# Kernel tuning notes

Measured on AMD Instinct MI355X. Metric: run time of the kernel, lower is better.

The kernel has to match this reference:

```python
import jax, jax.numpy as jnp
import numpy as np

TEMPERATURE = 8.0   # sqrt(d_k), d_k = 64
TOP_K = 5           # SparseAttention default top_k in mimicry/RIMs
EPS = 1e-7          # matches torch 10e-8


def _sparsify(attn_rows):
    """Per-row top-k sparsification: keep mass above the k-th largest value,
    clamp at zero, renormalize. attn_rows: [N, L]."""
    topk_vals = jax.lax.top_k(attn_rows, TOP_K)[0]          # [N, K]
    delta = topk_vals[:, -1:] + EPS                          # k-th largest per row
    w = jnp.maximum(attn_rows - delta, 0.0)                  # clamp(min=0)
    return w / (jnp.sum(w, axis=1, keepdims=True) + EPS)


def setup_inputs() -> dict:
    key = jax.random.key(0)
    kq, kk, kv = jax.random.split(key, 3)
    B, L, D = 4, 4096, 64
    q = jax.random.normal(kq, (B, L, D), dtype=jnp.float32)
    k = jax.random.normal(kk, (B, L, D), dtype=jnp.float32)
    v = jax.random.normal(kv, (B, L, D), dtype=jnp.float32)
    return {"q": q, "k": k, "v": v}


def reference(q, k, v):
    # attn = softmax(q k^T / temperature); dropout is identity in eval mode
    attn = jnp.einsum('bqd,bkd->bqk', q / TEMPERATURE, k)   # [B, Lq, Lk]
    attn = jax.nn.softmax(attn, axis=-1)
    B, Lq, Lk = attn.shape
    attn = _sparsify(attn.reshape(B * Lq, Lk)).reshape(B, Lq, Lk)
    out = jnp.einsum('bqk,bkd->bqd', attn, v)               # [B, Lq, Dv]
    return out, attn
```

## Files before the change

### kernel.cpp

```cpp
#include <hip/hip_runtime.h>
#include <math.h>

#define NB 4
#define L 4096
#define D 64
#define QPB 64
#define TCOLS 128
#define NT (L / TCOLS)

typedef __attribute__((ext_vector_type(8))) short short8;
typedef __attribute__((ext_vector_type(4))) float floatx4;
typedef unsigned int u32;

static __device__ inline ushort2 f2bf2(float x) {
    unsigned int u = __builtin_bit_cast(unsigned int, x);
    unsigned int uh = u + (0x7FFFu + ((u >> 16) & 1u));
    unsigned short h = (unsigned short)(uh >> 16);
    float hf = __builtin_bit_cast(float, (unsigned int)h << 16);
    float r = x - hf;
    unsigned int v = __builtin_bit_cast(unsigned int, r);
    unsigned short l = (unsigned short)((v + (0x7FFFu + ((v >> 16) & 1u))) >> 16);
    ushort2 p; p.x = h; p.y = l; return p;
}

static __device__ inline void dma16(const unsigned short* g, unsigned short* l) {
    __builtin_amdgcn_global_load_lds(
        (const __attribute__((address_space(1))) u32*)g,
        (__attribute__((address_space(3))) u32*)l, 16, 0, 0);
}

#define WS_QL 1048576
#define WS_KW 2097152

__global__ __launch_bounds__(256)
void convert_kernel(const float* __restrict__ qg, const float* __restrict__ kg,
                    unsigned short* __restrict__ ws) {
    unsigned int i = blockIdx.x * 256 + threadIdx.x;
    if (i < 262144) {
        float4 qv = ((const float4*)qg)[i];
        ushort2 p0 = f2bf2(qv.x), p1 = f2bf2(qv.y), p2 = f2bf2(qv.z), p3 = f2bf2(qv.w);
        ushort4 h; h.x = p0.x; h.y = p1.x; h.z = p2.x; h.w = p3.x;
        ushort4 l; l.x = p0.y; l.y = p1.y; l.z = p2.y; l.w = p3.y;
        *(ushort4*)&ws[i * 4] = h;
        *(ushort4*)&ws[WS_QL + i * 4] = l;
    } else {
        unsigned int j = i - 262144;
        float4 kv = ((const float4*)kg)[j];
        ushort2 p0 = f2bf2(kv.x), p1 = f2bf2(kv.y), p2 = f2bf2(kv.z), p3 = f2bf2(kv.w);
        ushort4 h; h.x = p0.x; h.y = p1.x; h.z = p2.x; h.w = p3.x;
        ushort4 l; l.x = p0.y; l.y = p1.y; l.z = p2.y; l.w = p3.y;
        unsigned int bcol = j >> 4;
        unsigned int f4   = j & 15;
        unsigned int tile = bcol >> 7;
        unsigned int tcol = bcol & 127;
        unsigned int cq   = f4 >> 1, half = f4 & 1;
        unsigned int base = tile * 16384 + (cq * 128 + tcol) * 8 + half * 4;
        *(ushort4*)&ws[WS_KW + base] = h;
        *(ushort4*)&ws[WS_KW + base + 8192] = l;
    }
}

__global__ __launch_bounds__(512, 2)
void sparse_attn_kernel(const unsigned short* __restrict__ ws,
                        const float* __restrict__ vg,
                        float* __restrict__ outg) {
    __shared__ unsigned short skt[2][16384];
    __shared__ float smv[QPB][5];
    __shared__ int   smc[QPB][5];
    __shared__ float smz[QPB];

    const int tid  = threadIdx.x;
    const int lane = tid & 63;
    const int w    = tid >> 6;
    const int rg   = w & 3;
    const int ch   = w >> 2;
    const int c16  = lane & 15;
    const int quad = lane >> 4;

    const int sblk  = (blockIdx.x & 7) * 32 + (blockIdx.x >> 3);
    const int qbase = sblk * QPB;
    const int b     = qbase >> 12;

    const unsigned short* qh = ws;
    const unsigned short* ql = ws + WS_QL;
    const unsigned short* kw = ws + WS_KW + (size_t)b * NT * 16384;

    const float* vb = vg + (size_t)b * L * D;
    float* attng = outg + (size_t)NB * L * D;
    float4* zrow = (float4*)(attng + (size_t)qbase * L);

    const int qrow = qbase + rg * 16 + c16;
    const short8 a0h = *(const short8*)&qh[(size_t)qrow * 64 + quad * 8];
    const short8 a1h = *(const short8*)&qh[(size_t)qrow * 64 + 32 + quad * 8];
    const short8 a0l = *(const short8*)&ql[(size_t)qrow * 64 + quad * 8];
    const short8 a1l = *(const short8*)&ql[(size_t)qrow * 64 + 32 + quad * 8];

#pragma unroll
    for (int jj = 0; jj < 4; ++jj) {
        int idx = w * 4 + jj;
        dma16(kw + idx * 512 + lane * 8, &skt[0][idx * 512]);
    }
    __syncthreads();

    float Z[4] = {0.f, 0.f, 0.f, 0.f};
    float tv[4][5];
    int   tc[4][5];
#pragma unroll
    for (int r = 0; r < 4; ++r)
#pragma unroll
        for (int i = 0; i < 5; ++i) { tv[r][i] = -INFINITY; tc[r][i] = -1; }

    for (int g = 0; g < NT; ++g) {
        if (g + 1 < NT) {
#pragma unroll
            for (int jj = 0; jj < 4; ++jj) {
                int idx = w * 4 + jj;
                dma16(kw + (g + 1) * 16384 + idx * 512 + lane * 8,
                      &skt[(g + 1) & 1][idx * 512]);
            }
        }

        const unsigned short* kbh = skt[g & 1];
        const unsigned short* kbl = skt[g & 1] + 8192;

#pragma unroll
        for (int j = 0; j < 4; ++j) {
            const int cg = ch * 4 + j;
            const int cb = cg * 16 + c16;
            short8 b0h = *(const short8*)&kbh[((quad)     * 128 + cb) * 8];
            short8 b1h = *(const short8*)&kbh[((4 + quad) * 128 + cb) * 8];
            short8 b0l = *(const short8*)&kbl[((quad)     * 128 + cb) * 8];
            short8 b1l = *(const short8*)&kbl[((4 + quad) * 128 + cb) * 8];
            floatx4 acc = {0.f, 0.f, 0.f, 0.f};
            acc = __builtin_amdgcn_mfma_f32_16x16x32_bf16(a0h, b0h, acc, 0, 0, 0);
            acc = __builtin_amdgcn_mfma_f32_16x16x32_bf16(a1h, b1h, acc, 0, 0, 0);
            acc = __builtin_amdgcn_mfma_f32_16x16x32_bf16(a0l, b0h, acc, 0, 0, 0);
            acc = __builtin_amdgcn_mfma_f32_16x16x32_bf16(a1l, b1h, acc, 0, 0, 0);
            acc = __builtin_amdgcn_mfma_f32_16x16x32_bf16(a0h, b0l, acc, 0, 0, 0);
            acc = __builtin_amdgcn_mfma_f32_16x16x32_bf16(a1h, b1l, acc, 0, 0, 0);
            const int col = g * TCOLS + cb;
#pragma unroll
            for (int r = 0; r < 4; ++r) {
                float s = acc[r] * 0.125f;
                Z[r] += __expf(s);
                bool q0 = s > tv[r][0];
                bool q1 = s > tv[r][1];
                bool q2 = s > tv[r][2];
                bool q3 = s > tv[r][3];
                bool q4 = s > tv[r][4];
                tv[r][4] = q4 ? (q3 ? tv[r][3] : s)   : tv[r][4];
                tc[r][4] = q4 ? (q3 ? tc[r][3] : col) : tc[r][4];
                tv[r][3] = q3 ? (q2 ? tv[r][2] : s)   : tv[r][3];
                tc[r][3] = q3 ? (q2 ? tc[r][2] : col) : tc[r][3];
                tv[r][2] = q2 ? (q1 ? tv[r][1] : s)   : tv[r][2];
                tc[r][2] = q2 ? (q1 ? tc[r][1] : col) : tc[r][2];
                tv[r][1] = q1 ? (q0 ? tv[r][0] : s)   : tv[r][1];
                tc[r][1] = q1 ? (q0 ? tc[r][0] : col) : tc[r][1];
                tv[r][0] = q0 ? s   : tv[r][0];
                tc[r][0] = q0 ? col : tc[r][0];
            }
        }

        float4 zv = make_float4(0.f, 0.f, 0.f, 0.f);
#pragma unroll
        for (int jj = 0; jj < 4; ++jj)
            zrow[(size_t)g * 2048 + jj * 512 + tid] = zv;

        __syncthreads();
    }

    float gv[4][5]; int gc[4][5]; float zz[4];
#pragma unroll
    for (int r = 0; r < 4; ++r) {
        float z = Z[r];
        z += __shfl_xor(z, 1, 64);
        z += __shfl_xor(z, 2, 64);
        z += __shfl_xor(z, 4, 64);
        z += __shfl_xor(z, 8, 64);
        zz[r] = z;
        const int rowl = rg * 16 + quad * 4 + r;
#pragma unroll
        for (int k5 = 0; k5 < 5; ++k5) {
            float cv = tv[r][0]; int cc = tc[r][0];
#pragma unroll
            for (int m = 8; m >= 1; m >>= 1) {
                float ov = __shfl_xor(cv, m, 64);
                int   oc = __shfl_xor(cc, m, 64);
                if (ov > cv || (ov == cv && oc < cc)) { cv = ov; cc = oc; }
            }
            gv[r][k5] = cv; gc[r][k5] = cc;
            if (ch == 1 && c16 == k5) { smv[rowl][k5] = cv; smc[rowl][k5] = cc; }
            if (tc[r][0] == cc) {
                tv[r][0] = tv[r][1]; tc[r][0] = tc[r][1];
                tv[r][1] = tv[r][2]; tc[r][1] = tc[r][2];
                tv[r][2] = tv[r][3]; tc[r][2] = tc[r][3];
                tv[r][3] = tv[r][4]; tc[r][3] = tc[r][4];
                tv[r][4] = -INFINITY; tc[r][4] = -1;
            }
        }
        if (ch == 1 && c16 == 5) smz[rowl] = z;
    }
    __syncthreads();

    if (ch == 0) {
#pragma unroll
        for (int r = 0; r < 4; ++r) {
            const int rowl = rg * 16 + quad * 4 + r;
            float z = zz[r] + smz[rowl];
#pragma unroll
            for (int f = 0; f < 5; ++f) {
                float fv = smv[rowl][f];
                int   fc = smc[rowl][f];
                bool q0 = fv > gv[r][0];
                bool q1 = fv > gv[r][1];
                bool q2 = fv > gv[r][2];
                bool q3 = fv > gv[r][3];
                bool q4 = fv > gv[r][4];
                gv[r][4] = q4 ? (q3 ? gv[r][3] : fv) : gv[r][4];
                gc[r][4] = q4 ? (q3 ? gc[r][3] : fc) : gc[r][4];
                gv[r][3] = q3 ? (q2 ? gv[r][2] : fv) : gv[r][3];
                gc[r][3] = q3 ? (q2 ? gc[r][2] : fc) : gc[r][3];
                gv[r][2] = q2 ? (q1 ? gv[r][1] : fv) : gv[r][2];
                gc[r][2] = q2 ? (q1 ? gc[r][1] : fc) : gc[r][2];
                gv[r][1] = q1 ? (q0 ? gv[r][0] : fv) : gv[r][1];
                gc[r][1] = q1 ? (q0 ? gc[r][0] : fc) : gc[r][1];
                gv[r][0] = q0 ? fv : gv[r][0];
                gc[r][0] = q0 ? fc : gc[r][0];
            }

            float invz = 1.0f / z;
            float e0 = __expf(gv[r][0]) * invz;
            float e1 = __expf(gv[r][1]) * invz;
            float e2 = __expf(gv[r][2]) * invz;
            float e3 = __expf(gv[r][3]) * invz;
            float e4 = __expf(gv[r][4]) * invz;
            float delta = e4 + 1e-7f;
            float w0 = fmaxf(e0 - delta, 0.f);
            float w1 = fmaxf(e1 - delta, 0.f);
            float w2 = fmaxf(e2 - delta, 0.f);
            float w3 = fmaxf(e3 - delta, 0.f);
            float inv = 1.0f / (w0 + w1 + w2 + w3 + 1e-7f);
            w0 *= inv; w1 *= inv; w2 *= inv; w3 *= inv;

            const int rowabs = qbase + rowl;

            const float4 v0 = *(const float4*)(vb + (size_t)gc[r][0] * D + c16 * 4);
            const float4 v1 = *(const float4*)(vb + (size_t)gc[r][1] * D + c16 * 4);
            const float4 v2 = *(const float4*)(vb + (size_t)gc[r][2] * D + c16 * 4);
            const float4 v3 = *(const float4*)(vb + (size_t)gc[r][3] * D + c16 * 4);
            float4 o;
            o.x = w0 * v0.x + w1 * v1.x + w2 * v2.x + w3 * v3.x;
            o.y = w0 * v0.y + w1 * v1.y + w2 * v2.y + w3 * v3.y;
            o.z = w0 * v0.z + w1 * v1.z + w2 * v2.z + w3 * v3.z;
            o.w = w0 * v0.w + w1 * v1.w + w2 * v2.w + w3 * v3.w;
            *(float4*)(outg + (size_t)rowabs * D + c16 * 4) = o;

            if (c16 < 4) {
                float wv = c16 == 0 ? w0 : c16 == 1 ? w1 : c16 == 2 ? w2 : w3;
                int   cs = c16 == 0 ? gc[r][0] : c16 == 1 ? gc[r][1]
                         : c16 == 2 ? gc[r][2] : gc[r][3];
                attng[(size_t)rowabs * L + cs] = wv;
            }
        }
    }
}

extern "C" void kernel_launch(void* const* d_in, const int* in_sizes, int n_in,
                              void* d_out, int out_size, void* d_ws, size_t ws_size,
                              hipStream_t stream) {
    const float* q = (const float*)d_in[0];
    const float* k = (const float*)d_in[1];
    const float* v = (const float*)d_in[2];
    float* out = (float*)d_out;
    unsigned short* ws = (unsigned short*)d_ws;

    convert_kernel<<<2048, 256, 0, stream>>>(q, k, ws);

    dim3 grid(NB * L / QPB);
    sparse_attn_kernel<<<grid, 512, 0, stream>>>(ws, v, out);
}
```

Before: 346.5 us.

## Drop softmax denominator via exp ratio, read K directly from global, shrink blocks

Folds log2(e)/temperature into Q during conversion so scores come out in log2 units. The sparsified weights are then computed as (2^(s_i - s_5) - 1) normalized, which removes the per-element exp and row-sum accumulation entirely. The shared-memory K double buffer is replaced with direct global loads from a K layout with per-batch column-major chunks. Blocks shrink to 16 query rows with four waves splitting the columns, followed by an LDS merge of the per-wave top-5 lists. This drops per-element exp and index bookkeeping and barriers, but relies on cache hits for K reuse and changes the EPS semantics slightly.

Result: faster. 334.9 us (-3.4%).

```diff
diff --git a/kernel.cpp b/kernel.cpp
--- a/kernel.cpp
+++ b/kernel.cpp
@@ -4,13 +4,14 @@
 #define NB 4
 #define L 4096
 #define D 64
-#define QPB 64
-#define TCOLS 128
-#define NT (L / TCOLS)
+#define WS_QL 1048576
+#define WS_K  2097152
+#define KBS   524288
+#define KPL   262144
+#define QSCALE 0.1803368801111243f
 
 typedef __attribute__((ext_vector_type(8))) short short8;
 typedef __attribute__((ext_vector_type(4))) float floatx4;
-typedef unsigned int u32;
 
 static __device__ inline ushort2 f2bf2(float x) {
     unsigned int u = __builtin_bit_cast(unsigned int, x);
@@ -23,22 +24,14 @@
     ushort2 p; p.x = h; p.y = l; return p;
 }
 
-static __device__ inline void dma16(const unsigned short* g, unsigned short* l) {
-    __builtin_amdgcn_global_load_lds(
-        (const __attribute__((address_space(1))) u32*)g,
-        (__attribute__((address_space(3))) u32*)l, 16, 0, 0);
-}
-
-#define WS_QL 1048576
-#define WS_KW 2097152
-
 __global__ __launch_bounds__(256)
 void convert_kernel(const float* __restrict__ qg, const float* __restrict__ kg,
                     unsigned short* __restrict__ ws) {
     unsigned int i = blockIdx.x * 256 + threadIdx.x;
     if (i < 262144) {
         float4 qv = ((const float4*)qg)[i];
-        ushort2 p0 = f2bf2(qv.x), p1 = f2bf2(qv.y), p2 = f2bf2(qv.z), p3 = f2bf2(qv.w);
+        ushort2 p0 = f2bf2(qv.x * QSCALE), p1 = f2bf2(qv.y * QSCALE),
+                p2 = f2bf2(qv.z * QSCALE), p3 = f2bf2(qv.w * QSCALE);
         ushort4 h; h.x = p0.x; h.y = p1.x; h.z = p2.x; h.w = p3.x;
         ushort4 l; l.x = p0.y; l.y = p1.y; l.z = p2.y; l.w = p3.y;
         *(ushort4*)&ws[i * 4] = h;
@@ -51,136 +44,106 @@
         ushort4 l; l.x = p0.y; l.y = p1.y; l.z = p2.y; l.w = p3.y;
         unsigned int bcol = j >> 4;
         unsigned int f4   = j & 15;
-        unsigned int tile = bcol >> 7;
-        unsigned int tcol = bcol & 127;
+        unsigned int b    = bcol >> 12, col = bcol & 4095;
         unsigned int cq   = f4 >> 1, half = f4 & 1;
-        unsigned int base = tile * 16384 + (cq * 128 + tcol) * 8 + half * 4;
-        *(ushort4*)&ws[WS_KW + base] = h;
-        *(ushort4*)&ws[WS_KW + base + 8192] = l;
-    }
-}
-
-__global__ __launch_bounds__(512, 2)
+        size_t base = WS_K + (size_t)b * KBS + ((size_t)cq * 4096 + col) * 8 + half * 4;
+        *(ushort4*)&ws[base] = h;
+        *(ushort4*)&ws[base + KPL] = l;
+    }
+}
+
+#define SENT 0x7FFFFFFF
+
+__global__ __launch_bounds__(256, 4)
 void sparse_attn_kernel(const unsigned short* __restrict__ ws,
                         const float* __restrict__ vg,
                         float* __restrict__ outg) {
-    __shared__ unsigned short skt[2][16384];
-    __shared__ float smv[QPB][5];
-    __shared__ int   smc[QPB][5];
-    __shared__ float smz[QPB];
+    __shared__ float smv[3][16][5];
+    __shared__ int   smc[3][16][4];
 
     const int tid  = threadIdx.x;
     const int lane = tid & 63;
-    const int w    = tid >> 6;
-    const int rg   = w & 3;
-    const int ch   = w >> 2;
+    const int wid  = tid >> 6;
     const int c16  = lane & 15;
     const int quad = lane >> 4;
 
-    const int sblk  = (blockIdx.x & 7) * 32 + (blockIdx.x >> 3);
-    const int qbase = sblk * QPB;
+    const int sblk  = (blockIdx.x & 7) * 128 + (blockIdx.x >> 3);
+    const int qbase = sblk * 16;
     const int b     = qbase >> 12;
 
-    const unsigned short* qh = ws;
-    const unsigned short* ql = ws + WS_QL;
-    const unsigned short* kw = ws + WS_KW + (size_t)b * NT * 16384;
-
+    const unsigned short* qh   = ws;
+    const unsigned short* ql   = ws + WS_QL;
+    const unsigned short* kbat = ws + WS_K + (size_t)b * KBS;
     const float* vb = vg + (size_t)b * L * D;
     float* attng = outg + (size_t)NB * L * D;
-    float4* zrow = (float4*)(attng + (size_t)qbase * L);
-
-    const int qrow = qbase + rg * 16 + c16;
+
+    const int qrow = qbase + c16;
     const short8 a0h = *(const short8*)&qh[(size_t)qrow * 64 + quad * 8];
     const short8 a1h = *(const short8*)&qh[(size_t)qrow * 64 + 32 + quad * 8];
     const short8 a0l = *(const short8*)&ql[(size_t)qrow * 64 + quad * 8];
     const short8 a1l = *(const short8*)&ql[(size_t)qrow * 64 + 32 + quad * 8];
 
-#pragma unroll
-    for (int jj = 0; jj < 4; ++jj) {
-        int idx = w * 4 + jj;
-        dma16(kw + idx * 512 + lane * 8, &skt[0][idx * 512]);
-    }
-    __syncthreads();
-
-    float Z[4] = {0.f, 0.f, 0.f, 0.f};
     float tv[4][5];
-    int   tc[4][5];
-#pragma unroll
-    for (int r = 0; r < 4; ++r)
-#pragma unroll
-        for (int i = 0; i < 5; ++i) { tv[r][i] = -INFINITY; tc[r][i] = -1; }
-
-    for (int g = 0; g < NT; ++g) {
-        if (g + 1 < NT) {
-#pragma unroll
-            for (int jj = 0; jj < 4; ++jj) {
-                int idx = w * 4 + jj;
-                dma16(kw + (g + 1) * 16384 + idx * 512 + lane * 8,
-                      &skt[(g + 1) & 1][idx * 512]);
-            }
-        }
-
-        const unsigned short* kbh = skt[g & 1];
-        const unsigned short* kbl = skt[g & 1] + 8192;
-
-#pragma unroll
-        for (int j = 0; j < 4; ++j) {
-            const int cg = ch * 4 + j;
-            const int cb = cg * 16 + c16;
-            short8 b0h = *(const short8*)&kbh[((quad)     * 128 + cb) * 8];
-            short8 b1h = *(const short8*)&kbh[((4 + quad) * 128 + cb) * 8];
-            short8 b0l = *(const short8*)&kbl[((quad)     * 128 + cb) * 8];
-            short8 b1l = *(const short8*)&kbl[((4 + quad) * 128 + cb) * 8];
-            floatx4 acc = {0.f, 0.f, 0.f, 0.f};
-            acc = __builtin_amdgcn_mfma_f32_16x16x32_bf16(a0h, b0h, acc, 0, 0, 0);
-            acc = __builtin_amdgcn_mfma_f32_16x16x32_bf16(a1h, b1h, acc, 0, 0, 0);
-            acc = __builtin_amdgcn_mfma_f32_16x16x32_bf16(a0l, b0h, acc, 0, 0, 0);
-            acc = __builtin_amdgcn_mfma_f32_16x16x32_bf16(a1l, b1h, acc, 0, 0, 0);
-            acc = __builtin_amdgcn_mfma_f32_16x16x32_bf16(a0h, b0l, acc, 0, 0, 0);
-            acc = __builtin_amdgcn_mfma_f32_16x16x32_bf16(a1h, b1l, acc, 0, 0, 0);
-            const int col = g * TCOLS + cb;
-#pragma unroll
-            for (int r = 0; r < 4; ++r) {
-                float s = acc[r] * 0.125f;
-                Z[r] += __expf(s);
-                bool q0 = s > tv[r][0];
-                bool q1 = s > tv[r][1];
-                bool q2 = s > tv[r][2];
-                bool q3 = s > tv[r][3];
-                bool q4 = s > tv[r][4];
-                tv[r][4] = q4 ? (q3 ? tv[r][3] : s)   : tv[r][4];
-                tc[r][4] = q4 ? (q3 ? tc[r][3] : col) : tc[r][4];
-                tv[r][3] = q3 ? (q2 ? tv[r][2] : s)   : tv[r][3];
-                tc[r][3] = q3 ? (q2 ? tc[r][2] : col) : tc[r][3];
-                tv[r][2] = q2 ? (q1 ? tv[r][1] : s)   : tv[r][2];
-                tc[r][2] = q2 ? (q1 ? tc[r][1] : col) : tc[r][2];
-                tv[r][1] = q1 ? (q0 ? tv[r][0] : s)   : tv[r][1];
-                tc[r][1] = q1 ? (q0 ? tc[r][0] : col) : tc[r][1];
-                tv[r][0] = q0 ? s   : tv[r][0];
-                tc[r][0] = q0 ? col : tc[r][0];
-            }
-        }
-
-        float4 zv = make_float4(0.f, 0.f, 0.f, 0.f);
-#pragma unroll
-        for (int jj = 0; jj < 4; ++jj)
-            zrow[(size_t)g * 2048 + jj * 512 + tid] = zv;
-
-        __syncthreads();
-    }
-
-    float gv[4][5]; int gc[4][5]; float zz[4];
+    int   tc[4][4];
 #pragma unroll
     for (int r = 0; r < 4; ++r) {
-        float z = Z[r];
-        z += __shfl_xor(z, 1, 64);
-        z += __shfl_xor(z, 2, 64);
-        z += __shfl_xor(z, 4, 64);
-        z += __shfl_xor(z, 8, 64);
-        zz[r] = z;
-        const int rowl = rg * 16 + quad * 4 + r;
-#pragma unroll
-        for (int k5 = 0; k5 < 5; ++k5) {
+#pragma unroll
+        for (int i = 0; i < 5; ++i) tv[r][i] = -INFINITY;
+#pragma unroll
+        for (int i = 0; i < 4; ++i) tc[r][i] = SENT;
+    }
+
+    const int colq = wid * 1024;
+    const unsigned short* bp0 = kbat + ((size_t)(quad)     * 4096 + colq + c16) * 8;
+    const unsigned short* bp1 = kbat + ((size_t)(4 + quad) * 4096 + colq + c16) * 8;
+    const float4 zv = make_float4(0.f, 0.f, 0.f, 0.f);
+
+#pragma unroll 4
+    for (int cg = 0; cg < 64; ++cg) {
+        const int off = cg * 128;
+        short8 b0h = *(const short8*)(bp0 + off);
+        short8 b1h = *(const short8*)(bp1 + off);
+        short8 b0l = *(const short8*)(bp0 + KPL + off);
+        short8 b1l = *(const short8*)(bp1 + KPL + off);
+        floatx4 acc = {0.f, 0.f, 0.f, 0.f};
+        acc = __builtin_amdgcn_mfma_f32_16x16x32_bf16(a0h, b0h, acc, 0, 0, 0);
+        acc = __builtin_amdgcn_mfma_f32_16x16x32_bf16(a1h, b1h, acc, 0, 0, 0);
+        acc = __builtin_amdgcn_mfma_f32_16x16x32_bf16(a0l, b0h, acc, 0, 0, 0);
+        acc = __builtin_amdgcn_mfma_f32_16x16x32_bf16(a1l, b1h, acc, 0, 0, 0);
+        acc = __builtin_amdgcn_mfma_f32_16x16x32_bf16(a0h, b0l, acc, 0, 0, 0);
+        acc = __builtin_amdgcn_mfma_f32_16x16x32_bf16(a1h, b1l, acc, 0, 0, 0);
+
+        {
+            int idx = cg * 64 + lane;
+            *(float4*)&attng[(size_t)(qbase + (idx >> 8)) * L + colq + (idx & 255) * 4] = zv;
+        }
+
+        const int col = colq + cg * 16 + c16;
+#pragma unroll
+        for (int r = 0; r < 4; ++r) {
+            float s = acc[r];
+            bool q0 = s > tv[r][0];
+            bool q1 = s > tv[r][1];
+            bool q2 = s > tv[r][2];
+            bool q3 = s > tv[r][3];
+            bool q4 = s > tv[r][4];
+            tv[r][4] = q4 ? (q3 ? tv[r][3] : s)   : tv[r][4];
+            tv[r][3] = q3 ? (q2 ? tv[r][2] : s)   : tv[r][3];
+            tc[r][3] = q3 ? (q2 ? tc[r][2] : col) : tc[r][3];
+            tv[r][2] = q2 ? (q1 ? tv[r][1] : s)   : tv[r][2];
+            tc[r][2] = q2 ? (q1 ? tc[r][1] : col) : tc[r][2];
+            tv[r][1] = q1 ? (q0 ? tv[r][0] : s)   : tv[r][1];
+            tc[r][1] = q1 ? (q0 ? tc[r][0] : col) : tc[r][1];
+            tv[r][0] = q0 ? s   : tv[r][0];
+            tc[r][0] = q0 ? col : tc[r][0];
+        }
+    }
+
+    float gv[4][5]; int gc[4][4];
+#pragma unroll
+    for (int r = 0; r < 4; ++r) {
+#pragma unroll
+        for (int k5 = 0; k5 < 4; ++k5) {
             float cv = tv[r][0]; int cc = tc[r][0];
 #pragma unroll
             for (int m = 8; m >= 1; m >>= 1) {
@@ -189,65 +152,97 @@
                 if (ov > cv || (ov == cv && oc < cc)) { cv = ov; cc = oc; }
             }
             gv[r][k5] = cv; gc[r][k5] = cc;
-            if (ch == 1 && c16 == k5) { smv[rowl][k5] = cv; smc[rowl][k5] = cc; }
-            if (tc[r][0] == cc) {
+            if (tc[r][0] == cc && tv[r][0] == cv) {
                 tv[r][0] = tv[r][1]; tc[r][0] = tc[r][1];
                 tv[r][1] = tv[r][2]; tc[r][1] = tc[r][2];
                 tv[r][2] = tv[r][3]; tc[r][2] = tc[r][3];
-                tv[r][3] = tv[r][4]; tc[r][3] = tc[r][4];
-                tv[r][4] = -INFINITY; tc[r][4] = -1;
-            }
-        }
-        if (ch == 1 && c16 == 5) smz[rowl] = z;
+                tv[r][3] = tv[r][4]; tc[r][3] = SENT;
+                tv[r][4] = -INFINITY;
+            }
+        }
+        float fv = tv[r][0];
+#pragma unroll
+        for (int m = 8; m >= 1; m >>= 1) fv = fmaxf(fv, __shfl_xor(fv, m, 64));
+        gv[r][4] = fv;
+    }
+
+    if (wid > 0) {
+#pragma unroll
+        for (int r = 0; r < 4; ++r) {
+            const int rowl = quad * 4 + r;
+            if (c16 < 4) {
+                smv[wid - 1][rowl][c16] = gv[r][c16];
+                smc[wid - 1][rowl][c16] = gc[r][c16];
+            } else if (c16 == 4) {
+                smv[wid - 1][rowl][4] = gv[r][4];
+            }
+        }
     }
     __syncthreads();
 
-    if (ch == 0) {
+    if (wid == 0) {
 #pragma unroll
         for (int r = 0; r < 4; ++r) {
-            const int rowl = rg * 16 + quad * 4 + r;
-            float z = zz[r] + smz[rowl];
-#pragma unroll
-            for (int f = 0; f < 5; ++f) {
-                float fv = smv[rowl][f];
-                int   fc = smc[rowl][f];
-                bool q0 = fv > gv[r][0];
-                bool q1 = fv > gv[r][1];
-                bool q2 = fv > gv[r][2];
-                bool q3 = fv > gv[r][3];
-                bool q4 = fv > gv[r][4];
-                gv[r][4] = q4 ? (q3 ? gv[r][3] : fv) : gv[r][4];
-                gc[r][4] = q4 ? (q3 ? gc[r][3] : fc) : gc[r][4];
-                gv[r][3] = q3 ? (q2 ? gv[r][2] : fv) : gv[r][3];
-                gc[r][3] = q3 ? (q2 ? gc[r][2] : fc) : gc[r][3];
-                gv[r][2] = q2 ? (q1 ? gv[r][1] : fv) : gv[r][2];
-                gc[r][2] = q2 ? (q1 ? gc[r][1] : fc) : gc[r][2];
-                gv[r][1] = q1 ? (q0 ? gv[r][0] : fv) : gv[r][1];
-                gc[r][1] = q1 ? (q0 ? gc[r][0] : fc) : gc[r][1];
-                gv[r][0] = q0 ? fv : gv[r][0];
-                gc[r][0] = q0 ? fc : gc[r][0];
-            }
-
-            float invz = 1.0f / z;
-            float e0 = __expf(gv[r][0]) * invz;
-            float e1 = __expf(gv[r][1]) * invz;
-            float e2 = __expf(gv[r][2]) * invz;
-            float e3 = __expf(gv[r][3]) * invz;
-            float e4 = __expf(gv[r][4]) * invz;
-            float delta = e4 + 1e-7f;
-            float w0 = fmaxf(e0 - delta, 0.f);
-            float w1 = fmaxf(e1 - delta, 0.f);
-            float w2 = fmaxf(e2 - delta, 0.f);
-            float w3 = fmaxf(e3 - delta, 0.f);
-            float inv = 1.0f / (w0 + w1 + w2 + w3 + 1e-7f);
-            w0 *= inv; w1 *= inv; w2 *= inv; w3 *= inv;
+            const int rowl = quad * 4 + r;
+            float lv[5]; int lc[4];
+#pragma unroll
+            for (int i = 0; i < 5; ++i) lv[i] = gv[r][i];
+#pragma unroll
+            for (int i = 0; i < 4; ++i) lc[i] = gc[r][i];
+
+#pragma unroll
+            for (int f = 0; f < 3; ++f) {
+#pragma unroll
+                for (int s5 = 0; s5 < 4; ++s5) {
+                    float v = smv[f][rowl][s5];
+                    int   c = smc[f][rowl][s5];
+                    bool q0 = v > lv[0];
+                    bool q1 = v > lv[1];
+                    bool q2 = v > lv[2];
+                    bool q3 = v > lv[3];
+                    bool q4 = v > lv[4];
+                    lv[4] = q4 ? (q3 ? lv[3] : v) : lv[4];
+                    lv[3] = q3 ? (q2 ? lv[2] : v) : lv[3];
+                    lc[3] = q3 ? (q2 ? lc[2] : c) : lc[3];
+                    lv[2] = q2 ? (q1 ? lv[1] : v) : lv[2];
+                    lc[2] = q2 ? (q1 ? lc[1] : c) : lc[2];
+                    lv[1] = q1 ? (q0 ? lv[0] : v) : lv[1];
+                    lc[1] = q1 ? (q0 ? lc[0] : c) : lc[1];
+                    lv[0] = q0 ? v : lv[0];
+                    lc[0] = q0 ? c : lc[0];
+                }
+                {
+                    float v = smv[f][rowl][4];
+                    bool q0 = v > lv[0];
+                    bool q1 = v > lv[1];
+                    bool q2 = v > lv[2];
+                    bool q3 = v > lv[3];
+                    bool q4 = v > lv[4];
+                    lv[4] = q4 ? (q3 ? lv[3] : v) : lv[4];
+                    lv[3] = q3 ? (q2 ? lv[2] : v) : lv[3];
+                    lv[2] = q2 ? (q1 ? lv[1] : v) : lv[2];
+                    lv[1] = q1 ? (q0 ? lv[0] : v) : lv[1];
+                    lv[0] = q0 ? v : lv[0];
+                }
+            }
+
+            float u0 = exp2f(lv[0] - lv[4]) - 1.0f;
+            float u1 = exp2f(lv[1] - lv[4]) - 1.0f;
+            float u2 = exp2f(lv[2] - lv[4]) - 1.0f;
+            float u3 = exp2f(lv[3] - lv[4]) - 1.0f;
+            float inv = 1.0f / (u0 + u1 + u2 + u3 + 1e-30f);
+            float w0 = u0 * inv, w1 = u1 * inv, w2 = u2 * inv, w3 = u3 * inv;
 
             const int rowabs = qbase + rowl;
 
-            const float4 v0 = *(const float4*)(vb + (size_t)gc[r][0] * D + c16 * 4);
-            const float4 v1 = *(const float4*)(vb + (size_t)gc[r][1] * D + c16 * 4);
-            const float4 v2 = *(const float4*)(vb + (size_t)gc[r][2] * D + c16 * 4);
-            const float4 v3 = *(const float4*)(vb + (size_t)gc[r][3] * D + c16 * 4);
+            unsigned int i0 = min((unsigned)lc[0], 4095u);
+            unsigned int i1 = min((unsigned)lc[1], 4095u);
+            unsigned int i2 = min((unsigned)lc[2], 4095u);
+            unsigned int i3 = min((unsigned)lc[3], 4095u);
+            const float4 v0 = *(const float4*)(vb + (size_t)i0 * D + c16 * 4);
+            const float4 v1 = *(const float4*)(vb + (size_t)i1 * D + c16 * 4);
+            const float4 v2 = *(const float4*)(vb + (size_t)i2 * D + c16 * 4);
+            const float4 v3 = *(const float4*)(vb + (size_t)i3 * D + c16 * 4);
             float4 o;
             o.x = w0 * v0.x + w1 * v1.x + w2 * v2.x + w3 * v3.x;
             o.y = w0 * v0.y + w1 * v1.y + w2 * v2.y + w3 * v3.y;
@@ -257,9 +252,10 @@
 
             if (c16 < 4) {
                 float wv = c16 == 0 ? w0 : c16 == 1 ? w1 : c16 == 2 ? w2 : w3;
-                int   cs = c16 == 0 ? gc[r][0] : c16 == 1 ? gc[r][1]
-                         : c16 == 2 ? gc[r][2] : gc[r][3];
-                attng[(size_t)rowabs * L + cs] = wv;
+                int   cs = c16 == 0 ? lc[0] : c16 == 1 ? lc[1]
+                         : c16 == 2 ? lc[2] : lc[3];
+                if ((unsigned)cs < 4096u && wv > 0.f)
+                    attng[(size_t)rowabs * L + cs] = wv;
             }
         }
     }
@@ -276,6 +272,5 @@
 
     convert_kernel<<<2048, 256, 0, stream>>>(q, k, ws);
 
-    dim3 grid(NB * L / QPB);
-    sparse_attn_kernel<<<grid, 512, 0, stream>>>(ws, v, out);
-}
+    sparse_attn_kernel<<<1024, 256, 0, stream>>>(ws, v, out);
+}
```
